# Optimization experiments

Hardware: AMD Instinct MI355X
Metric: run time of the kernel (lower is better)

The kernel has to match this reference:

```python
import jax, jax.numpy as jnp
import numpy as np

N, B, T, I, H = 16, 16, 512, 256, 512


def setup_inputs() -> dict:
    key = jax.random.key(0)
    k1, k2, k3, k4, k5 = jax.random.split(key, 5)
    stdv = 1.0 / np.sqrt(H)
    x = jax.random.normal(k1, (N, B, T, I), dtype=jnp.float32)
    w_ih = jax.random.uniform(k2, (N, H, I), minval=-stdv, maxval=stdv, dtype=jnp.float32)
    w_hh = jax.random.uniform(k3, (N, H, H), minval=-stdv, maxval=stdv, dtype=jnp.float32)
    b_ih = jax.random.uniform(k4, (N, H), minval=-stdv, maxval=stdv, dtype=jnp.float32)
    b_hh = jax.random.uniform(k5, (N, H), minval=-stdv, maxval=stdv, dtype=jnp.float32)
    return {"x": x, "w_ih": w_ih, "w_hh": w_hh, "b_ih": b_ih, "b_hh": b_hh}


def reference(x, w_ih, w_hh, b_ih, b_hh):
    # Fused input projection for all timesteps: [N,B,T,H]
    x_proj = jnp.einsum('nbti,nhi->nbth', x, w_ih) + b_ih[:, None, None, :]
    x_proj_t = jnp.moveaxis(x_proj, 2, 0)  # [T,N,B,H] for scan over time
    h0 = jnp.zeros((N, B, H), dtype=x.dtype)
    bhh = b_hh[:, None, :]  # [N,1,H]

    def step(h, xt):
        h_proj = jnp.einsum('nbh,noh->nbo', h, w_hh) + bhh
        h_new = jnp.tanh(xt + h_proj)
        return h_new, h_new

    h_n, ys = jax.lax.scan(step, h0, x_proj_t)  # ys: [T,N,B,H]
    output = jnp.moveaxis(ys, 0, 2)  # [N,B,T,H]
    return output, h_n
```

## Files before the change

### kernel.cpp

```cpp
#include <hip/hip_runtime.h>
#include <hip/hip_fp16.h>

#define NN 16
#define BB 16
#define TT 512
#define II 256
#define HH 512

typedef _Float16 half2_t __attribute__((ext_vector_type(2)));

#if defined(__has_builtin)
#  if __has_builtin(__builtin_amdgcn_fdot2)
#    define USE_FDOT2 1
#  endif
#endif

__device__ __forceinline__ float fdot2(half2_t a, half2_t b, float c) {
#ifdef USE_FDOT2
    return __builtin_amdgcn_fdot2(a, b, c, false);
#else
    return c + (float)a[0] * (float)b[0] + (float)a[1] * (float)b[1];
#endif
}

__device__ __forceinline__ half2_t bch(unsigned u) {
    return __builtin_bit_cast(half2_t, u);
}

__global__ __launch_bounds__(256, 3) void k1_xproj(
    const float* __restrict__ x,
    const float* __restrict__ w_ih,
    const float* __restrict__ b_ih,
    const float* __restrict__ b_hh,
    float* __restrict__ pre)
{
    __shared__ half2_t A2[128][65];
    __shared__ half2_t B2[64][65];

    const int tid = threadIdx.x;
    const int n   = blockIdx.z;
    const int bt0 = blockIdx.x * 128;
    const int h0  = blockIdx.y * 64;

    const float* xa = x    + ((size_t)n * (BB * TT) + bt0) * II;
    const float* wb = w_ih + ((size_t)n * HH + h0) * II;

    const int tx = tid & 15;
    const int ty = tid >> 4;

    float acc[8][4] = {};

    for (int kc = 0; kc < 2; ++kc) {
        #pragma unroll
        for (int rep = 0; rep < 16; ++rep) {
            int flat = rep * 256 + tid;
            int row  = flat >> 5;
            int c4   = flat & 31;
            float4 v = reinterpret_cast<const float4*>(xa + (size_t)row * II + kc * 128)[c4];
            A2[row][c4 * 2]     = half2_t{(_Float16)v.x, (_Float16)v.y};
            A2[row][c4 * 2 + 1] = half2_t{(_Float16)v.z, (_Float16)v.w};
        }
        #pragma unroll
        for (int rep = 0; rep < 8; ++rep) {
            int flat = rep * 256 + tid;
            int row  = flat >> 5;
            int c4   = flat & 31;
            float4 w = reinterpret_cast<const float4*>(wb + (size_t)row * II + kc * 128)[c4];
            B2[row][c4 * 2]     = half2_t{(_Float16)w.x, (_Float16)w.y};
            B2[row][c4 * 2 + 1] = half2_t{(_Float16)w.z, (_Float16)w.w};
        }
        __syncthreads();

        #pragma unroll
        for (int k2 = 0; k2 < 64; k2 += 2) {
            half2_t a0[8][2], b0[4][2];
            #pragma unroll
            for (int r = 0; r < 8; ++r) {
                a0[r][0] = A2[ty * 8 + r][k2];
                a0[r][1] = A2[ty * 8 + r][k2 + 1];
            }
            #pragma unroll
            for (int c = 0; c < 4; ++c) {
                b0[c][0] = B2[tx * 4 + c][k2];
                b0[c][1] = B2[tx * 4 + c][k2 + 1];
            }
            #pragma unroll
            for (int r = 0; r < 8; ++r)
                #pragma unroll
                for (int c = 0; c < 4; ++c)
                    acc[r][c] = fdot2(a0[r][1], b0[c][1],
                                fdot2(a0[r][0], b0[c][0], acc[r][c]));
        }
        __syncthreads();
    }

    float bias[4];
    #pragma unroll
    for (int c = 0; c < 4; ++c) {
        int h = h0 + tx * 4 + c;
        bias[c] = b_ih[n * HH + h] + b_hh[n * HH + h];
    }

    float* prow = pre + ((size_t)n * (BB * TT) + bt0) * HH + h0;
    #pragma unroll
    for (int r = 0; r < 8; ++r) {
        float4 ov;
        ov.x = acc[r][0] + bias[0];
        ov.y = acc[r][1] + bias[1];
        ov.z = acc[r][2] + bias[2];
        ov.w = acc[r][3] + bias[3];
        *reinterpret_cast<float4*>(prow + (size_t)(ty * 8 + r) * HH + tx * 4) = ov;
    }
}

#define LREG 96
#define K2_LDS (1024 + 4096 + 16 * 1024 * 8)

__global__ __launch_bounds__(1024, 4) void k2_rnn(
    const float* __restrict__ w_hh,
    float* __restrict__ out,
    float* __restrict__ hn)
{
    extern __shared__ char smem[];
    _Float16* h1   = (_Float16*)smem;
    float* partial = (float*)(smem + 1024);
    uint2* wlds    = (uint2*)(smem + 1024 + 4096);

    const int tid = threadIdx.x;
    const int o   = tid & (HH - 1);
    const int kh  = tid >> 9;
    const int n   = blockIdx.x >> 4;
    const int b   = blockIdx.x & 15;

    const float* wrow = w_hh + ((size_t)(n * HH + o)) * HH + kh * 256;

    half2_t wr[LREG];
    #pragma unroll
    for (int j = 0; j < 48; ++j) {
        float4 v = reinterpret_cast<const float4*>(wrow)[j];
        wr[2 * j]     = half2_t{(_Float16)v.x, (_Float16)v.y};
        wr[2 * j + 1] = half2_t{(_Float16)v.z, (_Float16)v.w};
    }
    #pragma unroll
    for (int j = 0; j < 16; ++j) {
        float4 v = reinterpret_cast<const float4*>(wrow + 192)[j];
        uint2 u;
        u.x = __builtin_bit_cast(unsigned, half2_t{(_Float16)v.x, (_Float16)v.y});
        u.y = __builtin_bit_cast(unsigned, half2_t{(_Float16)v.z, (_Float16)v.w});
        wlds[j * 1024 + tid] = u;
    }

    float* mybase = out + ((size_t)(n * BB + b)) * TT * HH + o;

    if (tid < HH) h1[tid] = (_Float16)0.f;
    float pre_next = 0.f;
    if (tid < HH) pre_next = mybase[0];
    __syncthreads();

    float hlast = 0.f;
    for (int t = 0; t < TT; ++t) {
        const uint4* hv = reinterpret_cast<const uint4*>(h1 + kh * 256);
        float acc0 = 0.f, acc1 = 0.f;
        #pragma unroll
        for (int j = 0; j < 24; ++j) {
            uint4 hq = hv[j];
            acc0 = fdot2(wr[4 * j + 0], bch(hq.x), acc0);
            acc1 = fdot2(wr[4 * j + 1], bch(hq.y), acc1);
            acc0 = fdot2(wr[4 * j + 2], bch(hq.z), acc0);
            acc1 = fdot2(wr[4 * j + 3], bch(hq.w), acc1);
        }
        #pragma unroll
        for (int j = 0; j < 8; ++j) {
            uint4 hq = hv[24 + j];
            uint2 w0 = wlds[(2 * j) * 1024 + tid];
            uint2 w1 = wlds[(2 * j + 1) * 1024 + tid];
            acc0 = fdot2(bch(w0.x), bch(hq.x), acc0);
            acc1 = fdot2(bch(w0.y), bch(hq.y), acc1);
            acc0 = fdot2(bch(w1.x), bch(hq.z), acc0);
            acc1 = fdot2(bch(w1.y), bch(hq.w), acc1);
        }
        partial[tid] = acc0 + acc1;
        __syncthreads();
        if (tid < HH) {
            float s = pre_next + partial[tid] + partial[tid + HH];
            s = fminf(fmaxf(s, -15.f), 15.f);
            float e = __expf(2.0f * s);
            float v = (e - 1.0f) / (e + 1.0f);
            mybase[(size_t)t * HH] = v;
            h1[o] = (_Float16)v;
            hlast = v;
            if (t + 1 < TT) pre_next = mybase[(size_t)(t + 1) * HH];
        }
        __syncthreads();
    }

    if (tid < HH) hn[((size_t)(n * BB + b)) * HH + o] = hlast;
}

extern "C" void kernel_launch(void* const* d_in, const int* in_sizes, int n_in,
                              void* d_out, int out_size, void* d_ws, size_t ws_size,
                              hipStream_t stream) {
    const float* x    = (const float*)d_in[0];
    const float* w_ih = (const float*)d_in[1];
    const float* w_hh = (const float*)d_in[2];
    const float* b_ih = (const float*)d_in[3];
    const float* b_hh = (const float*)d_in[4];

    float* out = (float*)d_out;
    float* hn  = out + (size_t)NN * BB * TT * HH;

    dim3 g1(64, 8, 16);
    hipLaunchKernelGGL(k1_xproj, g1, dim3(256), 0, stream, x, w_ih, b_ih, b_hh, out);

    hipFuncSetAttribute(reinterpret_cast<const void*>(k2_rnn),
                        hipFuncAttributeMaxDynamicSharedMemorySize, K2_LDS);
    hipLaunchKernelGGL(k2_rnn, dim3(NN * BB), dim3(1024), K2_LDS, stream,
                       w_hh, out, hn);
}
```

Measured before the change: 1.659 ms.

## Use MFMA for input projection and shuffle-reduce RNN step with double-buffered h

The input-projection GEMM moves from fdot2 scalar math to 16x16x32 f16 MFMA instructions with 128x128 tiles and padded LDS rows. The recurrent kernel now interleaves the two K-halves across adjacent lanes, so it reduces them with a shuffle instead of an LDS partial-sum exchange. It also double-buffers h, which leaves one barrier per timestep instead of two. The risk is that per-element scalar stores in k1 are less coalesced, and every thread now computes tanh redundantly.

```diff
diff --git a/kernel.cpp b/kernel.cpp
--- a/kernel.cpp
+++ b/kernel.cpp
@@ -8,6 +8,8 @@
 #define HH 512
 
 typedef _Float16 half2_t __attribute__((ext_vector_type(2)));
+typedef _Float16 f16x8  __attribute__((ext_vector_type(8)));
+typedef float    f32x4  __attribute__((ext_vector_type(4)));
 
 #if defined(__has_builtin)
 #  if __has_builtin(__builtin_amdgcn_fdot2)
@@ -26,29 +28,45 @@
 __device__ __forceinline__ half2_t bch(unsigned u) {
     return __builtin_bit_cast(half2_t, u);
 }
-
-__global__ __launch_bounds__(256, 3) void k1_xproj(
+__device__ __forceinline__ unsigned hcb(half2_t h) {
+    return __builtin_bit_cast(unsigned, h);
+}
+
+#define K1_LDA 136
+#define K1_LDS_BYTES (2 * 128 * K1_LDA * 2)
+
+__global__ __launch_bounds__(256, 2) void k1_xproj(
     const float* __restrict__ x,
     const float* __restrict__ w_ih,
     const float* __restrict__ b_ih,
     const float* __restrict__ b_hh,
     float* __restrict__ pre)
 {
-    __shared__ half2_t A2[128][65];
-    __shared__ half2_t B2[64][65];
+    extern __shared__ char smem[];
+    _Float16* A2 = (_Float16*)smem;
+    _Float16* B2 = (_Float16*)smem + 128 * K1_LDA;
 
     const int tid = threadIdx.x;
     const int n   = blockIdx.z;
-    const int bt0 = blockIdx.x * 128;
-    const int h0  = blockIdx.y * 64;
+    const int h0  = blockIdx.x * 128;
+    const int bt0 = blockIdx.y * 128;
 
     const float* xa = x    + ((size_t)n * (BB * TT) + bt0) * II;
     const float* wb = w_ih + ((size_t)n * HH + h0) * II;
 
-    const int tx = tid & 15;
-    const int ty = tid >> 4;
-
-    float acc[8][4] = {};
+    const int lane = tid & 63;
+    const int wid  = tid >> 6;
+    const int wr   = (wid >> 1) * 64;
+    const int wc   = (wid & 1) * 64;
+    const int l15  = lane & 15;
+    const int kb   = (lane >> 4) * 8;
+
+    f32x4 acc[4][4];
+    #pragma unroll
+    for (int m = 0; m < 4; ++m)
+        #pragma unroll
+        for (int c = 0; c < 4; ++c)
+            acc[m][c] = (f32x4){0.f, 0.f, 0.f, 0.f};
 
     for (int kc = 0; kc < 2; ++kc) {
         #pragma unroll
@@ -57,64 +75,60 @@
             int row  = flat >> 5;
             int c4   = flat & 31;
             float4 v = reinterpret_cast<const float4*>(xa + (size_t)row * II + kc * 128)[c4];
-            A2[row][c4 * 2]     = half2_t{(_Float16)v.x, (_Float16)v.y};
-            A2[row][c4 * 2 + 1] = half2_t{(_Float16)v.z, (_Float16)v.w};
-        }
-        #pragma unroll
-        for (int rep = 0; rep < 8; ++rep) {
-            int flat = rep * 256 + tid;
-            int row  = flat >> 5;
-            int c4   = flat & 31;
+            uint2 ua;
+            ua.x = hcb(half2_t{(_Float16)v.x, (_Float16)v.y});
+            ua.y = hcb(half2_t{(_Float16)v.z, (_Float16)v.w});
+            *reinterpret_cast<uint2*>(&A2[row * K1_LDA + c4 * 4]) = ua;
+
             float4 w = reinterpret_cast<const float4*>(wb + (size_t)row * II + kc * 128)[c4];
-            B2[row][c4 * 2]     = half2_t{(_Float16)w.x, (_Float16)w.y};
-            B2[row][c4 * 2 + 1] = half2_t{(_Float16)w.z, (_Float16)w.w};
+            uint2 uw;
+            uw.x = hcb(half2_t{(_Float16)w.x, (_Float16)w.y});
+            uw.y = hcb(half2_t{(_Float16)w.z, (_Float16)w.w});
+            *reinterpret_cast<uint2*>(&B2[row * K1_LDA + c4 * 4]) = uw;
         }
         __syncthreads();
 
         #pragma unroll
-        for (int k2 = 0; k2 < 64; k2 += 2) {
-            half2_t a0[8][2], b0[4][2];
-            #pragma unroll
-            for (int r = 0; r < 8; ++r) {
-                a0[r][0] = A2[ty * 8 + r][k2];
-                a0[r][1] = A2[ty * 8 + r][k2 + 1];
-            }
-            #pragma unroll
-            for (int c = 0; c < 4; ++c) {
-                b0[c][0] = B2[tx * 4 + c][k2];
-                b0[c][1] = B2[tx * 4 + c][k2 + 1];
-            }
-            #pragma unroll
-            for (int r = 0; r < 8; ++r)
+        for (int kk = 0; kk < 4; ++kk) {
+            f16x8 af[4], bf[4];
+            #pragma unroll
+            for (int m = 0; m < 4; ++m)
+                af[m] = *reinterpret_cast<const f16x8*>(
+                    &A2[(wr + m * 16 + l15) * K1_LDA + kk * 32 + kb]);
+            #pragma unroll
+            for (int c = 0; c < 4; ++c)
+                bf[c] = *reinterpret_cast<const f16x8*>(
+                    &B2[(wc + c * 16 + l15) * K1_LDA + kk * 32 + kb]);
+            #pragma unroll
+            for (int m = 0; m < 4; ++m)
                 #pragma unroll
                 for (int c = 0; c < 4; ++c)
-                    acc[r][c] = fdot2(a0[r][1], b0[c][1],
-                                fdot2(a0[r][0], b0[c][0], acc[r][c]));
+                    acc[m][c] = __builtin_amdgcn_mfma_f32_16x16x32_f16(
+                        af[m], bf[c], acc[m][c], 0, 0, 0);
         }
         __syncthreads();
     }
 
+    const int crow = (lane >> 4) * 4;
     float bias[4];
     #pragma unroll
     for (int c = 0; c < 4; ++c) {
-        int h = h0 + tx * 4 + c;
+        int h = h0 + wc + c * 16 + l15;
         bias[c] = b_ih[n * HH + h] + b_hh[n * HH + h];
     }
-
     float* prow = pre + ((size_t)n * (BB * TT) + bt0) * HH + h0;
     #pragma unroll
-    for (int r = 0; r < 8; ++r) {
-        float4 ov;
-        ov.x = acc[r][0] + bias[0];
-        ov.y = acc[r][1] + bias[1];
-        ov.z = acc[r][2] + bias[2];
-        ov.w = acc[r][3] + bias[3];
-        *reinterpret_cast<float4*>(prow + (size_t)(ty * 8 + r) * HH + tx * 4) = ov;
-    }
+    for (int m = 0; m < 4; ++m)
+        #pragma unroll
+        for (int c = 0; c < 4; ++c)
+            #pragma unroll
+            for (int r = 0; r < 4; ++r)
+                prow[(size_t)(wr + m * 16 + crow + r) * HH + wc + c * 16 + l15]
+                    = acc[m][c][r] + bias[c];
 }
 
 #define LREG 96
-#define K2_LDS (1024 + 4096 + 16 * 1024 * 8)
+#define K2_LDS (2 * 1024 + 16 * 1024 * 8)
 
 __global__ __launch_bounds__(1024, 4) void k2_rnn(
     const float* __restrict__ w_hh,
@@ -122,13 +136,12 @@
     float* __restrict__ hn)
 {
     extern __shared__ char smem[];
-    _Float16* h1   = (_Float16*)smem;
-    float* partial = (float*)(smem + 1024);
-    uint2* wlds    = (uint2*)(smem + 1024 + 4096);
+    _Float16* hb = (_Float16*)smem;
+    uint2* wlds  = (uint2*)(smem + 2048);
 
     const int tid = threadIdx.x;
-    const int o   = tid & (HH - 1);
-    const int kh  = tid >> 9;
+    const int o   = tid >> 1;
+    const int kh  = tid & 1;
     const int n   = blockIdx.x >> 4;
     const int b   = blockIdx.x & 15;
 
@@ -145,21 +158,21 @@
     for (int j = 0; j < 16; ++j) {
         float4 v = reinterpret_cast<const float4*>(wrow + 192)[j];
         uint2 u;
-        u.x = __builtin_bit_cast(unsigned, half2_t{(_Float16)v.x, (_Float16)v.y});
-        u.y = __builtin_bit_cast(unsigned, half2_t{(_Float16)v.z, (_Float16)v.w});
+        u.x = hcb(half2_t{(_Float16)v.x, (_Float16)v.y});
+        u.y = hcb(half2_t{(_Float16)v.z, (_Float16)v.w});
         wlds[j * 1024 + tid] = u;
     }
 
     float* mybase = out + ((size_t)(n * BB + b)) * TT * HH + o;
 
-    if (tid < HH) h1[tid] = (_Float16)0.f;
-    float pre_next = 0.f;
-    if (tid < HH) pre_next = mybase[0];
+    hb[tid] = (_Float16)0.f;
+    float pre_next = mybase[0];
     __syncthreads();
 
     float hlast = 0.f;
+    int p = 0;
     for (int t = 0; t < TT; ++t) {
-        const uint4* hv = reinterpret_cast<const uint4*>(h1 + kh * 256);
+        const uint4* hv = reinterpret_cast<const uint4*>(hb + p * 512 + kh * 256);
         float acc0 = 0.f, acc1 = 0.f;
         #pragma unroll
         for (int j = 0; j < 24; ++j) {
@@ -179,22 +192,23 @@
             acc0 = fdot2(bch(w1.x), bch(hq.z), acc0);
             acc1 = fdot2(bch(w1.y), bch(hq.w), acc1);
         }
-        partial[tid] = acc0 + acc1;
+        float s = acc0 + acc1;
+        s += __shfl_xor(s, 1);
+        s += pre_next;
+        s = fminf(fmaxf(s, -15.f), 15.f);
+        float e = __expf(2.0f * s);
+        float v = (e - 1.0f) / (e + 1.0f);
+        if (kh == 0) {
+            hb[(p ^ 1) * 512 + o] = (_Float16)v;
+            mybase[(size_t)t * HH] = v;
+        }
+        hlast = v;
+        if (t + 1 < TT) pre_next = mybase[(size_t)(t + 1) * HH];
         __syncthreads();
-        if (tid < HH) {
-            float s = pre_next + partial[tid] + partial[tid + HH];
-            s = fminf(fmaxf(s, -15.f), 15.f);
-            float e = __expf(2.0f * s);
-            float v = (e - 1.0f) / (e + 1.0f);
-            mybase[(size_t)t * HH] = v;
-            h1[o] = (_Float16)v;
-            hlast = v;
-            if (t + 1 < TT) pre_next = mybase[(size_t)(t + 1) * HH];
-        }
-        __syncthreads();
-    }
-
-    if (tid < HH) hn[((size_t)(n * BB + b)) * HH + o] = hlast;
+        p ^= 1;
+    }
+
+    if (kh == 0) hn[((size_t)(n * BB + b)) * HH + o] = hlast;
 }
 
 extern "C" void kernel_launch(void* const* d_in, const int* in_sizes, int n_in,
@@ -209,8 +223,10 @@
     float* out = (float*)d_out;
     float* hn  = out + (size_t)NN * BB * TT * HH;
 
-    dim3 g1(64, 8, 16);
-    hipLaunchKernelGGL(k1_xproj, g1, dim3(256), 0, stream, x, w_ih, b_ih, b_hh, out);
+    hipFuncSetAttribute(reinterpret_cast<const void*>(k1_xproj),
+                        hipFuncAttributeMaxDynamicSharedMemorySize, K1_LDS_BYTES);
+    hipLaunchKernelGGL(k1_xproj, dim3(4, 64, 16), dim3(256), K1_LDS_BYTES, stream,
+                       x, w_ih, b_ih, b_hh, out);
 
     hipFuncSetAttribute(reinterpret_cast<const void*>(k2_rnn),
                         hipFuncAttributeMaxDynamicSharedMemorySize, K2_LDS);
```

Result: slower. 1.866 ms (+12.5%).
